# Kernel tuning notes

Measured on AMD Instinct MI355X. Metric: run time of the kernel, lower is better.

The kernel has to match this reference:

```python
import jax, jax.numpy as jnp
from jax import lax
import numpy as np

# ViT-Base / Violin config
P = 16; IMG = 224; C = 768; H = 12; DEPTH = 12
S = 14; NPATCH = S * S            # 196
N = NPATCH + 1                    # 197 with cls token
HID = 4 * C; NCLS = 1000; BATCH = 32
NUM_CURVES = 6
EPS = 1e-5


def _curve_inv_indices(S):
    """Inverse permutations (patch position -> position along curve) for the 6 curves.
    's'  = row-wise snake (boustrophedon), 'h' = column-wise snake, 'm' = anti-diagonal zigzag;
    '*r' = reversed traversal. (Original repo's compute_curve_order helpers were not in the
    provided source; these are faithful stand-ins with the same structure: permutations of 0..195.)"""
    NP_ = S * S
    grid = np.arange(NP_).reshape(S, S)
    orders = {}
    snake = grid.copy(); snake[1::2] = snake[1::2, ::-1]
    orders['s'] = snake.reshape(-1)
    col = grid.T.copy(); col[1::2] = col[1::2, ::-1]
    orders['h'] = col.reshape(-1)
    diag = []
    for d in range(2 * S - 1):
        coords = [(i, d - i) for i in range(max(0, d - S + 1), min(d, S - 1) + 1)]
        if d % 2:
            coords = coords[::-1]
        diag += [grid[i, j] for i, j in coords]
    orders['m'] = np.array(diag)
    for c in ['s', 'h', 'm']:
        orders[c + 'r'] = orders[c][::-1].copy()
    inv = []
    for c in ['s', 'sr', 'h', 'hr', 'm', 'mr']:
        v = np.empty(NP_, np.int32)
        v[orders[c]] = np.arange(NP_, dtype=np.int32)
        inv.append(v)
    return np.stack(inv)  # (6, 196)


def _layernorm(x, w, b):
    m = jnp.mean(x, axis=-1, keepdims=True)
    v = jnp.mean(jnp.square(x - m), axis=-1, keepdims=True)
    return (x - m) / jnp.sqrt(v + EPS) * w + b


def setup_inputs() -> dict:
    key = jax.random.key(0)
    ks = jax.random.split(key, 24)
    rn = lambda k, sh: jax.random.normal(k, sh, jnp.float32) * 0.02
    d = {}
    d["images"] = jax.random.normal(ks[0], (BATCH, 3, IMG, IMG), jnp.float32)
    d["patch_w"] = rn(ks[1], (C, 3, P, P))
    d["patch_b"] = jnp.zeros((C,), jnp.float32)
    d["cls_token"] = rn(ks[2], (1, 1, C))
    d["pos_embed"] = rn(ks[3], (1, N, C))
    d["ln1_w"] = jnp.ones((DEPTH, C), jnp.float32)
    d["ln1_b"] = jnp.zeros((DEPTH, C), jnp.float32)
    d["qkv_w"] = rn(ks[4], (DEPTH, C, 3 * C))   # qkv_bias=False
    d["proj_w"] = rn(ks[5], (DEPTH, C, C))
    d["proj_b"] = jnp.zeros((DEPTH, C), jnp.float32)
    d["ai"] = jax.random.normal(ks[6], (DEPTH, NUM_CURVES, H), jnp.float32)  # torch.randn init
    d["ln2_w"] = jnp.ones((DEPTH, C), jnp.float32)
    d["ln2_b"] = jnp.zeros((DEPTH, C), jnp.float32)
    d["fc1_w"] = rn(ks[7], (DEPTH, C, HID))
    d["fc1_b"] = jnp.zeros((DEPTH, HID), jnp.float32)
    d["fc2_w"] = rn(ks[8], (DEPTH, HID, C))
    d["fc2_b"] = jnp.zeros((DEPTH, C), jnp.float32)
    d["norm_w"] = jnp.ones((C,), jnp.float32)
    d["norm_b"] = jnp.zeros((C,), jnp.float32)
    d["head_w"] = rn(ks[9], (C, NCLS))
    d["head_b"] = jnp.zeros((NCLS,), jnp.float32)
    d["curve_idx"] = jnp.asarray(_curve_inv_indices(S))  # int32 (6, 196)
    return d


def reference(images, patch_w, patch_b, cls_token, pos_embed,
              ln1_w, ln1_b, qkv_w, proj_w, proj_b, ai,
              ln2_w, ln2_b, fc1_w, fc1_b, fc2_w, fc2_b,
              norm_w, norm_b, head_w, head_b, curve_idx):
    B = images.shape[0]
    hd = C // H
    scale = hd ** -0.5
    # patch embed: Conv2d(3, C, k=16, s=16)
    x = lax.conv_general_dilated(images, patch_w, (P, P), 'VALID',
                                 dimension_numbers=('NCHW', 'OIHW', 'NCHW'))
    x = x + patch_b[None, :, None, None]
    x = x.reshape(B, C, NPATCH).transpose(0, 2, 1)          # (B, 196, C)
    x = jnp.concatenate([jnp.broadcast_to(cls_token, (B, 1, C)), x], axis=1)
    x = x + pos_embed                                        # (B, 197, C)

    # curve-distance tensors: |pos_c(p) - pos_c(q)| for each curve c -> (6, 196, 196)
    Dmat = jnp.abs(curve_idx[:, :, None] - curve_idx[:, None, :]).astype(jnp.float32)

    def block(x, p):
        l1w, l1b, qw, pw, pb, a, l2w, l2b, f1w, f1b, f2w, f2b = p
        h = _layernorm(x, l1w, l1b)
        qkv = (h @ qw).reshape(B, N, 3, H, hd).transpose(2, 0, 3, 1, 4)
        q, k, v = qkv[0], qkv[1], qkv[2]                     # (B, H, N, hd)
        attn = jnp.einsum('bhnd,bhmd->bhnm', q, k) * scale
        # multi-curve sigmoid-decay mask, averaged over curves
        sig = jax.nn.sigmoid(a)                              # (6, H)
        core = jnp.power(sig[:, :, None, None], Dmat[:, None, :, :]).mean(0)  # (H,196,196)
        M = jnp.ones((H, N, N), x.dtype).at[:, 1:, 1:].set(core)  # ones for cls row/col
        attn = jax.nn.softmax(attn * M[None], axis=-1)
        o = jnp.einsum('bhnm,bhmd->bhnd', attn, v)
        o = o.transpose(0, 2, 1, 3).reshape(B, N, C)
        x = x + o @ pw + pb
        h2 = _layernorm(x, l2w, l2b)
        h2 = jax.nn.gelu(h2 @ f1w + f1b, approximate=False) @ f2w + f2b
        return x + h2, None

    params = (ln1_w, ln1_b, qkv_w, proj_w, proj_b, ai,
              ln2_w, ln2_b, fc1_w, fc1_b, fc2_w, fc2_b)
    x, _ = lax.scan(block, x, params)
    x = _layernorm(x, norm_w, norm_b)
    return x[:, 0] @ head_w + head_b                          # (B, 1000)
```

## Files before the change

### kernel.cpp

```cpp
#include <hip/hip_runtime.h>
#include <hip/hip_bf16.h>

typedef unsigned int u32;
typedef unsigned short u16;
typedef __attribute__((ext_vector_type(8))) short sh8;
typedef __attribute__((ext_vector_type(4))) float f4;

#define B_   32
#define C_   768
#define H_   12
#define N_   197
#define NP_  196
#define S_   14
#define HID_ 3072
#define NCLS_ 1000
#define ROWS_ (B_ * N_)
#define PROWS_ (B_ * NP_)
#define NT_   13
#define NPAD_ 200

#define AS1(p) ((const __attribute__((address_space(1))) void*)(p))
#define AS3(p) ((__attribute__((address_space(3))) void*)(p))

__device__ __forceinline__ bool probe_bf16(const u32* p) { return p[0] == 0x3F803F80u; }

__device__ __forceinline__ float ldg_any(const void* p, long i, bool isbf) {
    return isbf ? __bfloat162float(((const __hip_bfloat16*)p)[i])
                : ((const float*)p)[i];
}
__device__ __forceinline__ float bfbits2f(u16 u) { return __uint_as_float(((u32)u) << 16); }
__device__ __forceinline__ u16 f2bfbits(float f) {
    __hip_bfloat16 h = __float2bfloat16(f);
    return *(u16*)&h;
}
__device__ __forceinline__ sh8 zero8() {
    sh8 z;
#pragma unroll
    for (int e = 0; e < 8; ++e) z[e] = 0;
    return z;
}

__global__ __launch_bounds__(256)
void im2col_k(const void* __restrict__ images, u16* __restrict__ out, const u32* probe) {
    bool isbf = probe_bf16(probe);
    long idx = (long)blockIdx.x * 256 + threadIdx.x;
    if (idx >= (long)PROWS_ * 768) return;
    int r = (int)(idx / 768), k = (int)(idx % 768);
    int b = r / NP_, p = r % NP_;
    int py = p / S_, px = p % S_;
    int ch = k / 256, rr = k % 256, ii = rr / 16, jj = rr % 16;
    long src = ((long)(b * 3 + ch) * 224 + (py * 16 + ii)) * 224 + (px * 16 + jj);
    out[idx] = f2bfbits(ldg_any(images, src, isbf));
}

__global__ __launch_bounds__(256)
void cast_k(const void* __restrict__ src, u16* __restrict__ dst, long n, const u32* probe) {
    bool isbf = probe_bf16(probe);
    long idx = (long)blockIdx.x * 256 + threadIdx.x;
    if (idx >= n) return;
    dst[idx] = f2bfbits(ldg_any(src, idx, isbf));
}

__global__ __launch_bounds__(256)
void transpose_k(const void* __restrict__ W, long w_off, int K, int N,
                 u16* __restrict__ out, const u32* probe) {
    bool isbf = probe_bf16(probe);
    __shared__ float tile[32][33];
    int tx = threadIdx.x & 31, ty = threadIdx.x >> 5;
    int n0 = blockIdx.x * 32, k0 = blockIdx.y * 32;
#pragma unroll
    for (int i = ty; i < 32; i += 8) {
        int k = k0 + i, n = n0 + tx;
        tile[i][tx] = (k < K && n < N) ? ldg_any(W, w_off + (long)k * N + n, isbf) : 0.f;
    }
    __syncthreads();
#pragma unroll
    for (int i = ty; i < 32; i += 8) {
        int n = n0 + i, k = k0 + tx;
        if (n < N && k < K) out[(long)n * K + k] = f2bfbits(tile[tx][i]);
    }
}

__global__ __launch_bounds__(256)
void cls_k(const void* __restrict__ cls, const void* __restrict__ pos,
           float* __restrict__ x, const u32* probe) {
    bool isbf = probe_bf16(probe);
    int idx = blockIdx.x * 256 + threadIdx.x;
    if (idx >= B_ * C_) return;
    int b = idx / C_, c = idx % C_;
    x[(long)b * N_ * C_ + c] = ldg_any(cls, c, isbf) + ldg_any(pos, c, isbf);
}

__global__ __launch_bounds__(256)
void gemm_bf16_k(const u16* __restrict__ A, int M, int K,
                 const u16* __restrict__ Bt, int N,
                 const void* __restrict__ bias, long bias_off, int has_bias,
                 void* __restrict__ Cp, int ldc, int epi,
                 const void* __restrict__ pos, const u32* __restrict__ probe) {
    __shared__ __align__(16) u16 As[128 * 64];
    __shared__ __align__(16) u16 Bs[128 * 64];
    const int tid = threadIdx.x;
    const int lane = tid & 63, wave = tid >> 6;
    const int wr = (wave >> 1) * 64, wc = (wave & 1) * 64;
    const int m0 = blockIdx.y * 128, n0 = blockIdx.x * 128;
    const int lm = lane & 15, quad = lane >> 4;

    const u16* ga[4];
    const u16* gb[4];
#pragma unroll
    for (int i = 0; i < 4; ++i) {
        int p = i * 256 + tid;
        int r = p >> 3, cslot = p & 7;
        int c = cslot ^ (r & 7);
        int ar = m0 + r; if (ar >= M) ar = M - 1;
        ga[i] = A  + (size_t)ar * K + c * 8;
        gb[i] = Bt + (size_t)(n0 + r) * K + c * 8;
    }

    f4 acc[4][4];
#pragma unroll
    for (int i = 0; i < 4; ++i)
#pragma unroll
        for (int j = 0; j < 4; ++j)
#pragma unroll
            for (int r = 0; r < 4; ++r) acc[i][j][r] = 0.f;

    for (int k0 = 0; k0 < K; k0 += 64) {
        __syncthreads();
#pragma unroll
        for (int i = 0; i < 4; ++i) {
            int p = i * 256 + tid;
            __builtin_amdgcn_global_load_lds(AS1(ga[i] + k0), AS3(As + p * 8), 16, 0, 0);
            __builtin_amdgcn_global_load_lds(AS1(gb[i] + k0), AS3(Bs + p * 8), 16, 0, 0);
        }
        __syncthreads();
#pragma unroll
        for (int ks = 0; ks < 2; ++ks) {
            sh8 af[4], bfv[4];
#pragma unroll
            for (int i = 0; i < 4; ++i) {
                int row = wr + i * 16 + lm;
                int ch = ks * 4 + quad;
                af[i] = *(const sh8*)(As + row * 64 + ((ch ^ (row & 7)) << 3));
                int col = wc + i * 16 + lm;
                bfv[i] = *(const sh8*)(Bs + col * 64 + ((ch ^ (col & 7)) << 3));
            }
#pragma unroll
            for (int i = 0; i < 4; ++i)
#pragma unroll
                for (int j = 0; j < 4; ++j)
                    acc[i][j] = __builtin_amdgcn_mfma_f32_16x16x32_bf16(af[i], bfv[j], acc[i][j], 0, 0, 0);
        }
    }

    const bool isbf = probe_bf16(probe);
#pragma unroll
    for (int j = 0; j < 4; ++j) {
        int col = n0 + wc + j * 16 + lm;
        float bv = has_bias ? ldg_any(bias, bias_off + col, isbf) : 0.f;
#pragma unroll
        for (int i = 0; i < 4; ++i) {
            int rbase = m0 + wr + i * 16 + quad * 4;
#pragma unroll
            for (int r = 0; r < 4; ++r) {
                int row = rbase + r;
                if (row >= M) continue;
                float v = acc[i][j][r] + bv;
                if (epi == 0) {
                    ((u16*)Cp)[(size_t)row * ldc + col] = f2bfbits(v);
                } else if (epi == 1) {
                    v = 0.5f * v * (1.f + erff(v * 0.70710678118654752f));
                    ((u16*)Cp)[(size_t)row * ldc + col] = f2bfbits(v);
                } else if (epi == 2) {
                    ((float*)Cp)[(size_t)row * ldc + col] += v;
                } else {
                    int b = row / NP_, p = row % NP_;
                    v += ldg_any(pos, (long)(1 + p) * C_ + col, isbf);
                    ((float*)Cp)[((size_t)b * N_ + 1 + p) * ldc + col] = v;
                }
            }
        }
    }
}

__global__ __launch_bounds__(256)
void ln_bf16_k(const float* __restrict__ x,
               const void* __restrict__ w, long w_off,
               const void* __restrict__ b, long b_off,
               u16* __restrict__ out, const u32* __restrict__ probe) {
    bool isbf = probe_bf16(probe);
    int lane = threadIdx.x & 63, wave = threadIdx.x >> 6;
    int row = blockIdx.x * 4 + wave;
    const float* xr = x + (size_t)row * C_;
    f4 v[3];
#pragma unroll
    for (int p = 0; p < 3; ++p) v[p] = *(const f4*)(xr + p * 256 + lane * 4);
    float s = 0.f, q = 0.f;
#pragma unroll
    for (int p = 0; p < 3; ++p)
#pragma unroll
        for (int e = 0; e < 4; ++e) { float t = v[p][e]; s += t; q += t * t; }
#pragma unroll
    for (int m = 32; m > 0; m >>= 1) { s += __shfl_xor(s, m); q += __shfl_xor(q, m); }
    float mean = s * (1.f / 768.f);
    float var = q * (1.f / 768.f) - mean * mean;
    float rstd = rsqrtf(var + 1e-5f);
    u16* orow = out + (size_t)row * C_;
#pragma unroll
    for (int p = 0; p < 3; ++p) {
        ushort4 ov;
        int c = p * 256 + lane * 4;
        ov.x = f2bfbits((v[p][0] - mean) * rstd * ldg_any(w, w_off + c + 0, isbf) + ldg_any(b, b_off + c + 0, isbf));
        ov.y = f2bfbits((v[p][1] - mean) * rstd * ldg_any(w, w_off + c + 1, isbf) + ldg_any(b, b_off + c + 1, isbf));
        ov.z = f2bfbits((v[p][2] - mean) * rstd * ldg_any(w, w_off + c + 2, isbf) + ldg_any(b, b_off + c + 2, isbf));
        ov.w = f2bfbits((v[p][3] - mean) * rstd * ldg_any(w, w_off + c + 3, isbf) + ldg_any(b, b_off + c + 3, isbf));
        *(ushort4*)(orow + c) = ov;
    }
}

__global__ __launch_bounds__(256)
void ln_k(const float* __restrict__ x, int row_stride,
          const void* __restrict__ w, long w_off,
          const void* __restrict__ b, long b_off,
          float* __restrict__ out, const u32* __restrict__ probe) {
    bool isbf = probe_bf16(probe);
    int tid = threadIdx.x;
    long row = (long)blockIdx.x * row_stride;
    const float* xr = x + row * C_;
    float v0 = xr[tid], v1 = xr[tid + 256], v2 = xr[tid + 512];
    __shared__ float rs[256], rq[256];
    rs[tid] = v0 + v1 + v2;
    rq[tid] = v0 * v0 + v1 * v1 + v2 * v2;
    __syncthreads();
    for (int st = 128; st > 0; st >>= 1) {
        if (tid < st) { rs[tid] += rs[tid + st]; rq[tid] += rq[tid + st]; }
        __syncthreads();
    }
    float mean = rs[0] * (1.f / 768.f);
    float var = rq[0] * (1.f / 768.f) - mean * mean;
    float rstd = rsqrtf(var + 1e-5f);
    float* orow = out + (long)blockIdx.x * C_;
    orow[tid]       = (v0 - mean) * rstd * ldg_any(w, w_off + tid, isbf)       + ldg_any(b, b_off + tid, isbf);
    orow[tid + 256] = (v1 - mean) * rstd * ldg_any(w, w_off + tid + 256, isbf) + ldg_any(b, b_off + tid + 256, isbf);
    orow[tid + 512] = (v2 - mean) * rstd * ldg_any(w, w_off + tid + 512, isbf) + ldg_any(b, b_off + tid + 512, isbf);
}

__global__ __launch_bounds__(256)
void mask_k(const void* __restrict__ ai, long ai_off, const int* __restrict__ ci,
            float* __restrict__ Mm, const u32* __restrict__ probe) {
    bool isbf = probe_bf16(probe);
    const int h = blockIdx.y;
    __shared__ float ls_s[6];
    __shared__ float pw[6][196];
    if (threadIdx.x < 6) {
        float a = ldg_any(ai, ai_off + threadIdx.x * H_ + h, isbf);
        ls_s[threadIdx.x] = logf(1.f / (1.f + expf(-a)));
    }
    __syncthreads();
    for (int idx = threadIdx.x; idx < 6 * 196; idx += 256) {
        int c = idx / 196, d = idx % 196;
        pw[c][d] = expf((float)d * ls_s[c]);
    }
    __syncthreads();
    int r = blockIdx.x * 256 + threadIdx.x;
    if (r >= N_ * N_) return;
    int i = r / N_, j = r % N_;
    float v;
    if (i == 0 || j == 0) {
        v = 0.125f;
    } else {
        float acc = 0.f;
#pragma unroll
        for (int c = 0; c < 6; ++c) {
            int D = abs(ci[c * NP_ + (i - 1)] - ci[c * NP_ + (j - 1)]);
            acc += pw[c][D];
        }
        v = acc * (0.125f / 6.f);
    }
    Mm[(size_t)h * N_ * N_ + r] = v;
}

__global__ __launch_bounds__(128)
void attn3_k(const u16* __restrict__ qkv, const float* __restrict__ Mm,
             u16* __restrict__ o) {
    __shared__ __align__(16) u16 Ks[208 * 64];
    __shared__ __align__(16) u16 Vt[64 * NPAD_];
    __shared__ __align__(16) u16 Ps[2 * 16 * NPAD_];
    const int h = blockIdx.x, b = blockIdx.y, tid = threadIdx.x;
    const int lane = tid & 63, wave = tid >> 6;
    const int lm = lane & 15, quad = lane >> 4;
    const size_t qkv_b = (size_t)b * N_ * 2304;

    for (int idx = tid; idx < 208 * 8; idx += 128) {
        int r = idx >> 3, c = idx & 7;
        uint4 kv = make_uint4(0u, 0u, 0u, 0u);
        if (r < N_) kv = *(const uint4*)(qkv + qkv_b + (size_t)r * 2304 + 768 + h * 64 + c * 8);
        *(uint4*)(Ks + r * 64 + ((c ^ (r & 7)) << 3)) = kv;
    }
#pragma unroll
    for (int rr = 0; rr < 2; ++rr) {
        int r = tid + rr * 128;
        if (r < NPAD_) {
            ushort vv[64];
            if (r < N_) {
                const u16* vsrc = qkv + qkv_b + (size_t)r * 2304 + 1536 + h * 64;
#pragma unroll
                for (int c = 0; c < 8; ++c) *(uint4*)&vv[c * 8] = *(const uint4*)(vsrc + c * 8);
            } else {
#pragma unroll
                for (int e = 0; e < 64; ++e) vv[e] = 0;
            }
#pragma unroll
            for (int d = 0; d < 64; ++d) Vt[d * NPAD_ + r] = vv[d];
        }
    }
    __syncthreads();

    u16* psw = Ps + wave * 16 * NPAD_;
    for (int rt = wave; rt < NT_; rt += 2) {
        sh8 qf[2];
        int qrow = rt * 16 + lm;
#pragma unroll
        for (int ks = 0; ks < 2; ++ks) {
            qf[ks] = (qrow < N_)
                ? *(const sh8*)(qkv + qkv_b + (size_t)qrow * 2304 + h * 64 + ks * 32 + quad * 8)
                : zero8();
        }
        f4 sacc[NT_];
#pragma unroll
        for (int ct = 0; ct < NT_; ++ct)
#pragma unroll
            for (int r = 0; r < 4; ++r) sacc[ct][r] = 0.f;
#pragma unroll
        for (int ct = 0; ct < NT_; ++ct) {
#pragma unroll
            for (int ks = 0; ks < 2; ++ks) {
                int krow = ct * 16 + lm;
                sh8 kf = *(const sh8*)(Ks + krow * 64 + (((ks * 4 + quad) ^ (krow & 7)) << 3));
                sacc[ct] = __builtin_amdgcn_mfma_f32_16x16x32_bf16(qf[ks], kf, sacc[ct], 0, 0, 0);
            }
        }
        float mx[4] = {-1e30f, -1e30f, -1e30f, -1e30f};
#pragma unroll
        for (int ct = 0; ct < NT_; ++ct) {
            int col = ct * 16 + lm;
            int colc = col < N_ ? col : N_ - 1;
#pragma unroll
            for (int r = 0; r < 4; ++r) {
                int row = rt * 16 + quad * 4 + r;
                int rowc = row < N_ ? row : N_ - 1;
                float mval = Mm[((size_t)h * N_ + rowc) * N_ + colc];
                float v = sacc[ct][r] * mval;
                if (col >= N_) v = -1e30f;
                sacc[ct][r] = v;
                mx[r] = fmaxf(mx[r], v);
            }
        }
#pragma unroll
        for (int m = 8; m > 0; m >>= 1)
#pragma unroll
            for (int r = 0; r < 4; ++r) mx[r] = fmaxf(mx[r], __shfl_xor(mx[r], m));
        float sm[4] = {0.f, 0.f, 0.f, 0.f};
#pragma unroll
        for (int ct = 0; ct < NT_; ++ct) {
            int col = ct * 16 + lm;
#pragma unroll
            for (int r = 0; r < 4; ++r) {
                float p = __expf(sacc[ct][r] - mx[r]);
                sm[r] += p;
                if (col < NPAD_) psw[(quad * 4 + r) * NPAD_ + col] = f2bfbits(p);
            }
        }
#pragma unroll
        for (int m = 8; m > 0; m >>= 1)
#pragma unroll
            for (int r = 0; r < 4; ++r) sm[r] += __shfl_xor(sm[r], m);
        float rden[4];
#pragma unroll
        for (int r = 0; r < 4; ++r) rden[r] = 1.f / sm[r];

        sh8 pf[7];
#pragma unroll
        for (int ms = 0; ms < 7; ++ms) {
            int cm = ms * 4 + quad;
            pf[ms] = (cm <= 24) ? *(const sh8*)(psw + lm * NPAD_ + cm * 8) : zero8();
        }
        f4 oacc[4];
#pragma unroll
        for (int dt = 0; dt < 4; ++dt)
#pragma unroll
            for (int r = 0; r < 4; ++r) oacc[dt][r] = 0.f;
#pragma unroll
        for (int dt = 0; dt < 4; ++dt) {
#pragma unroll
            for (int ms = 0; ms < 7; ++ms) {
                int cm = ms * 4 + quad;
                sh8 vf = (cm <= 24) ? *(const sh8*)(Vt + (dt * 16 + lm) * NPAD_ + cm * 8) : zero8();
                oacc[dt] = __builtin_amdgcn_mfma_f32_16x16x32_bf16(pf[ms], vf, oacc[dt], 0, 0, 0);
            }
        }
#pragma unroll
        for (int dt = 0; dt < 4; ++dt) {
#pragma unroll
            for (int r = 0; r < 4; ++r) {
                int row = rt * 16 + quad * 4 + r;
                if (row < N_)
                    o[((size_t)(b * N_) + row) * C_ + h * 64 + dt * 16 + lm] =
                        f2bfbits(oacc[dt][r] * rden[r]);
            }
        }
    }
}

__global__ __launch_bounds__(256)
void head_k(const float* __restrict__ A,
            const void* __restrict__ W,
            const void* __restrict__ bias,
            void* __restrict__ out, const u32* __restrict__ probe) {
    const bool isbf = probe_bf16(probe);
    const int m = blockIdx.y;
    const int n = blockIdx.x * 256 + threadIdx.x;
    __shared__ float a_s[C_];
    for (int k = threadIdx.x; k < C_; k += 256) a_s[k] = A[(long)m * C_ + k];
    __syncthreads();
    if (n >= NCLS_) return;
    float acc = 0.f;
    if (isbf) {
        const u16* Wb = (const u16*)W;
#pragma unroll 16
        for (int k = 0; k < C_; ++k) acc = fmaf(a_s[k], bfbits2f(Wb[(long)k * NCLS_ + n]), acc);
        acc += bfbits2f(((const u16*)bias)[n]);
        ((u16*)out)[(long)m * NCLS_ + n] = f2bfbits(acc);
    } else {
        const float* Wf = (const float*)W;
#pragma unroll 16
        for (int k = 0; k < C_; ++k) acc = fmaf(a_s[k], Wf[(long)k * NCLS_ + n], acc);
        acc += ((const float*)bias)[n];
        ((float*)out)[(long)m * NCLS_ + n] = acc;
    }
}

extern "C" void kernel_launch(void* const* d_in, const int* in_sizes, int n_in,
                              void* d_out, int out_size, void* d_ws, size_t ws_size,
                              hipStream_t stream) {
    const void* images  = d_in[0];
    const void* patch_w = d_in[1];
    const void* patch_b = d_in[2];
    const void* cls_tok = d_in[3];
    const void* pos_emb = d_in[4];
    const void* ln1_w   = d_in[5];
    const void* ln1_b   = d_in[6];
    const void* qkv_w   = d_in[7];
    const void* proj_w  = d_in[8];
    const void* proj_b  = d_in[9];
    const void* ai      = d_in[10];
    const void* ln2_w   = d_in[11];
    const void* ln2_b   = d_in[12];
    const void* fc1_w   = d_in[13];
    const void* fc1_b   = d_in[14];
    const void* fc2_w   = d_in[15];
    const void* fc2_b   = d_in[16];
    const void* norm_w  = d_in[17];
    const void* norm_b  = d_in[18];
    const void* head_w  = d_in[19];
    const void* head_b  = d_in[20];
    const int*  curve   = (const int*)d_in[21];
    const u32*  probe   = (const u32*)ln1_w;

    char* wsp = (char*)d_ws;
    size_t off = 0;
    auto alloc = [&](size_t bytes) -> void* {
        void* p = wsp + off;
        off += (bytes + 255) & ~(size_t)255;
        return p;
    };
    float* x    = (float*)alloc((size_t)ROWS_ * C_ * 4);
    u16*   hbuf = (u16*)alloc((size_t)ROWS_ * C_ * 2);
    u16*   big  = (u16*)alloc((size_t)ROWS_ * HID_ * 2);
    u16*   obuf = (u16*)alloc((size_t)ROWS_ * C_ * 2);
    float* mm   = (float*)alloc((size_t)H_ * N_ * N_ * 4);
    u16*   wT   = (u16*)alloc((size_t)HID_ * C_ * 2);
    u16*   pwT  = (u16*)alloc((size_t)C_ * C_ * 2);
    float* lnf  = (float*)alloc((size_t)B_ * C_ * 4);
    (void)ws_size; (void)in_sizes; (void)n_in; (void)out_size;

    const int MT = (ROWS_ + 127) / 128;

    im2col_k<<<((long)PROWS_ * 768 + 255) / 256, 256, 0, stream>>>(images, hbuf, probe);
    cast_k<<<(768 * 768 + 255) / 256, 256, 0, stream>>>(patch_w, pwT, (long)768 * 768, probe);
    cls_k<<<(B_ * C_ + 255) / 256, 256, 0, stream>>>(cls_tok, pos_emb, x, probe);
    {
        dim3 g(768 / 128, PROWS_ / 128);
        gemm_bf16_k<<<g, 256, 0, stream>>>(hbuf, PROWS_, 768, pwT, 768,
                                           patch_b, 0, 1, x, 768, 3, pos_emb, probe);
    }

    for (int l = 0; l < 12; ++l) {
        ln_bf16_k<<<ROWS_ / 4, 256, 0, stream>>>(x, ln1_w, (long)l * C_, ln1_b, (long)l * C_, hbuf, probe);
        transpose_k<<<dim3(2304 / 32, 768 / 32), 256, 0, stream>>>(qkv_w, (long)l * 768 * 2304, 768, 2304, wT, probe);
        {
            dim3 g(2304 / 128, MT);
            gemm_bf16_k<<<g, 256, 0, stream>>>(hbuf, ROWS_, 768, wT, 2304,
                                               nullptr, 0, 0, big, 2304, 0, nullptr, probe);
        }
        mask_k<<<dim3((N_ * N_ + 255) / 256, H_), 256, 0, stream>>>(ai, (long)l * 6 * H_, curve, mm, probe);
        attn3_k<<<dim3(H_, B_), 128, 0, stream>>>(big, mm, obuf);
        transpose_k<<<dim3(768 / 32, 768 / 32), 256, 0, stream>>>(proj_w, (long)l * 768 * 768, 768, 768, wT, probe);
        {
            dim3 g(768 / 128, MT);
            gemm_bf16_k<<<g, 256, 0, stream>>>(obuf, ROWS_, 768, wT, 768,
                                               proj_b, (long)l * 768, 1, x, 768, 2, nullptr, probe);
        }
        ln_bf16_k<<<ROWS_ / 4, 256, 0, stream>>>(x, ln2_w, (long)l * C_, ln2_b, (long)l * C_, hbuf, probe);
        transpose_k<<<dim3(3072 / 32, 768 / 32), 256, 0, stream>>>(fc1_w, (long)l * 768 * 3072, 768, 3072, wT, probe);
        {
            dim3 g(3072 / 128, MT);
            gemm_bf16_k<<<g, 256, 0, stream>>>(hbuf, ROWS_, 768, wT, 3072,
                                               fc1_b, (long)l * HID_, 1, big, 3072, 1, nullptr, probe);
        }
        transpose_k<<<dim3(768 / 32, 3072 / 32), 256, 0, stream>>>(fc2_w, (long)l * 3072 * 768, 3072, 768, wT, probe);
        {
            dim3 g(768 / 128, MT);
            gemm_bf16_k<<<g, 256, 0, stream>>>(big, ROWS_, 3072, wT, 768,
                                               fc2_b, (long)l * C_, 1, x, 768, 2, nullptr, probe);
        }
    }

    ln_k<<<B_, 256, 0, stream>>>(x, N_, norm_w, 0, norm_b, 0, lnf, probe);
    head_k<<<dim3((NCLS_ + 255) / 256, B_), 256, 0, stream>>>(lnf, head_w, head_b, d_out, probe);
}
```

Measured before the change: 4.629 ms.

## Double-buffer GEMM LDS tiles and remap workgroups across XCDs

The bf16 GEMM kernel now uses two LDS buffers for the A and B tiles. It prefetches the next K-slice with global_load_lds while MFMAs run on the current slice, so one of the two barriers per iteration is gone and load latency overlaps with compute. The workgroup index is also remapped so that consecutive tiles land on the same XCD, which should improve L2 reuse of shared A/B panels. The cost is twice the LDS per block (64 KB), which may lower occupancy.

```diff
diff --git a/kernel.cpp b/kernel.cpp
--- a/kernel.cpp
+++ b/kernel.cpp
@@ -97,12 +97,19 @@
                  const void* __restrict__ bias, long bias_off, int has_bias,
                  void* __restrict__ Cp, int ldc, int epi,
                  const void* __restrict__ pos, const u32* __restrict__ probe) {
-    __shared__ __align__(16) u16 As[128 * 64];
-    __shared__ __align__(16) u16 Bs[128 * 64];
+    __shared__ __align__(16) u16 As[2][128 * 64];
+    __shared__ __align__(16) u16 Bs[2][128 * 64];
     const int tid = threadIdx.x;
     const int lane = tid & 63, wave = tid >> 6;
     const int wr = (wave >> 1) * 64, wc = (wave & 1) * 64;
-    const int m0 = blockIdx.y * 128, n0 = blockIdx.x * 128;
+
+    const int gx = gridDim.x;
+    const int nwg = gx * gridDim.y;
+    const int lin = blockIdx.y * gx + blockIdx.x;
+    const int q = nwg >> 3, r8 = nwg & 7;
+    const int xcd = lin & 7, cidx = lin >> 3;
+    const int wgid = (xcd < r8 ? xcd * (q + 1) : r8 * (q + 1) + (xcd - r8) * q) + cidx;
+    const int m0 = (wgid / gx) * 128, n0 = (wgid % gx) * 128;
     const int lm = lane & 15, quad = lane >> 4;
 
     const u16* ga[4];
@@ -125,15 +132,26 @@
 #pragma unroll
             for (int r = 0; r < 4; ++r) acc[i][j][r] = 0.f;
 
+#pragma unroll
+    for (int i = 0; i < 4; ++i) {
+        int p = i * 256 + tid;
+        __builtin_amdgcn_global_load_lds(AS1(ga[i]), AS3(&As[0][p * 8]), 16, 0, 0);
+        __builtin_amdgcn_global_load_lds(AS1(gb[i]), AS3(&Bs[0][p * 8]), 16, 0, 0);
+    }
+
+    int cur = 0;
     for (int k0 = 0; k0 < K; k0 += 64) {
         __syncthreads();
-#pragma unroll
-        for (int i = 0; i < 4; ++i) {
-            int p = i * 256 + tid;
-            __builtin_amdgcn_global_load_lds(AS1(ga[i] + k0), AS3(As + p * 8), 16, 0, 0);
-            __builtin_amdgcn_global_load_lds(AS1(gb[i] + k0), AS3(Bs + p * 8), 16, 0, 0);
-        }
-        __syncthreads();
+        if (k0 + 64 < K) {
+#pragma unroll
+            for (int i = 0; i < 4; ++i) {
+                int p = i * 256 + tid;
+                __builtin_amdgcn_global_load_lds(AS1(ga[i] + k0 + 64), AS3(&As[cur ^ 1][p * 8]), 16, 0, 0);
+                __builtin_amdgcn_global_load_lds(AS1(gb[i] + k0 + 64), AS3(&Bs[cur ^ 1][p * 8]), 16, 0, 0);
+            }
+        }
+        const u16* Ac = As[cur];
+        const u16* Bc = Bs[cur];
 #pragma unroll
         for (int ks = 0; ks < 2; ++ks) {
             sh8 af[4], bfv[4];
@@ -141,9 +159,9 @@
             for (int i = 0; i < 4; ++i) {
                 int row = wr + i * 16 + lm;
                 int ch = ks * 4 + quad;
-                af[i] = *(const sh8*)(As + row * 64 + ((ch ^ (row & 7)) << 3));
+                af[i] = *(const sh8*)(Ac + row * 64 + ((ch ^ (row & 7)) << 3));
                 int col = wc + i * 16 + lm;
-                bfv[i] = *(const sh8*)(Bs + col * 64 + ((ch ^ (col & 7)) << 3));
+                bfv[i] = *(const sh8*)(Bc + col * 64 + ((ch ^ (col & 7)) << 3));
             }
 #pragma unroll
             for (int i = 0; i < 4; ++i)
@@ -151,6 +169,7 @@
                 for (int j = 0; j < 4; ++j)
                     acc[i][j] = __builtin_amdgcn_mfma_f32_16x16x32_bf16(af[i], bfv[j], acc[i][j], 0, 0, 0);
         }
+        cur ^= 1;
     }
 
     const bool isbf = probe_bf16(probe);
```

Result: no change. 4.575 ms (-1.2%).

## Batch weight transposes across layers and remap GEMM workgroups per XCD

Applied to the files above, without the earlier changes.

When the workspace is large enough, all 12 layers' weights are transposed and cast to bf16 up front with four 3D-grid launches, replacing the 48 per-layer transpose launches. Each layer's GEMM then reads its own pre-transposed slice. Separately, the GEMM now remaps its linear block index so consecutive tiles land on the same XCD, which is meant to improve L2 reuse. The cost is extra workspace, with a fallback to the old per-layer path when the workspace is too small.

```diff
diff --git a/kernel.cpp b/kernel.cpp
--- a/kernel.cpp
+++ b/kernel.cpp
@@ -82,6 +82,29 @@
 }
 
 __global__ __launch_bounds__(256)
+void transpose_all_k(const void* __restrict__ W, long lstride, int K, int N,
+                     u16* __restrict__ out, const u32* probe) {
+    bool isbf = probe_bf16(probe);
+    __shared__ float tile[32][33];
+    const int l = blockIdx.z;
+    const long w_off = (long)l * lstride;
+    u16* o = out + (long)l * (long)K * N;
+    int tx = threadIdx.x & 31, ty = threadIdx.x >> 5;
+    int n0 = blockIdx.x * 32, k0 = blockIdx.y * 32;
+#pragma unroll
+    for (int i = ty; i < 32; i += 8) {
+        int k = k0 + i, n = n0 + tx;
+        tile[i][tx] = (k < K && n < N) ? ldg_any(W, w_off + (long)k * N + n, isbf) : 0.f;
+    }
+    __syncthreads();
+#pragma unroll
+    for (int i = ty; i < 32; i += 8) {
+        int n = n0 + i, k = k0 + tx;
+        if (n < N && k < K) o[(long)n * K + k] = f2bfbits(tile[tx][i]);
+    }
+}
+
+__global__ __launch_bounds__(256)
 void cls_k(const void* __restrict__ cls, const void* __restrict__ pos,
            float* __restrict__ x, const u32* probe) {
     bool isbf = probe_bf16(probe);
@@ -102,7 +125,14 @@
     const int tid = threadIdx.x;
     const int lane = tid & 63, wave = tid >> 6;
     const int wr = (wave >> 1) * 64, wc = (wave & 1) * 64;
-    const int m0 = blockIdx.y * 128, n0 = blockIdx.x * 128;
+
+    const int gx = gridDim.x;
+    const int nwg = gx * gridDim.y;
+    const int lin = blockIdx.y * gx + blockIdx.x;
+    const int q = nwg >> 3, r8 = nwg & 7;
+    const int xcd = lin & 7, cidx = lin >> 3;
+    const int wgid = (xcd < r8 ? xcd * (q + 1) : r8 * (q + 1) + (xcd - r8) * q) + cidx;
+    const int m0 = (wgid / gx) * 128, n0 = (wgid % gx) * 128;
     const int lm = lane & 15, quad = lane >> 4;
 
     const u16* ga[4];
@@ -482,7 +512,19 @@
     u16*   wT   = (u16*)alloc((size_t)HID_ * C_ * 2);
     u16*   pwT  = (u16*)alloc((size_t)C_ * C_ * 2);
     float* lnf  = (float*)alloc((size_t)B_ * C_ * 4);
-    (void)ws_size; (void)in_sizes; (void)n_in; (void)out_size;
+
+    const size_t qkvT_sz  = (size_t)12 * 2304 * 768;
+    const size_t projT_sz = (size_t)12 * 768 * 768;
+    const size_t fc1T_sz  = (size_t)12 * 3072 * 768;
+    const size_t fc2T_sz  = (size_t)12 * 768 * 3072;
+    size_t off_backup = off;
+    u16* qkvT  = (u16*)alloc(qkvT_sz * 2);
+    u16* projT = (u16*)alloc(projT_sz * 2);
+    u16* fc1T  = (u16*)alloc(fc1T_sz * 2);
+    u16* fc2T  = (u16*)alloc(fc2T_sz * 2);
+    const bool batched = (off <= ws_size);
+    if (!batched) off = off_backup;
+    (void)in_sizes; (void)n_in; (void)out_size;
 
     const int MT = (ROWS_ + 127) / 128;
 
@@ -495,33 +537,49 @@
                                            patch_b, 0, 1, x, 768, 3, pos_emb, probe);
     }
 
+    if (batched) {
+        transpose_all_k<<<dim3(2304 / 32, 768 / 32, 12), 256, 0, stream>>>(qkv_w,  (long)768 * 2304, 768, 2304, qkvT,  probe);
+        transpose_all_k<<<dim3(768 / 32,  768 / 32, 12), 256, 0, stream>>>(proj_w, (long)768 * 768,  768, 768,  projT, probe);
+        transpose_all_k<<<dim3(3072 / 32, 768 / 32, 12), 256, 0, stream>>>(fc1_w,  (long)768 * 3072, 768, 3072, fc1T,  probe);
+        transpose_all_k<<<dim3(768 / 32, 3072 / 32, 12), 256, 0, stream>>>(fc2_w,  (long)3072 * 768, 3072, 768, fc2T,  probe);
+    }
+
     for (int l = 0; l < 12; ++l) {
+        const u16* wq = batched ? qkvT  + (size_t)l * 2304 * 768 : wT;
+        const u16* wp = batched ? projT + (size_t)l * 768 * 768  : wT;
+        const u16* w1 = batched ? fc1T  + (size_t)l * 3072 * 768 : wT;
+        const u16* w2 = batched ? fc2T  + (size_t)l * 768 * 3072 : wT;
+
         ln_bf16_k<<<ROWS_ / 4, 256, 0, stream>>>(x, ln1_w, (long)l * C_, ln1_b, (long)l * C_, hbuf, probe);
-        transpose_k<<<dim3(2304 / 32, 768 / 32), 256, 0, stream>>>(qkv_w, (long)l * 768 * 2304, 768, 2304, wT, probe);
+        if (!batched)
+            transpose_k<<<dim3(2304 / 32, 768 / 32), 256, 0, stream>>>(qkv_w, (long)l * 768 * 2304, 768, 2304, wT, probe);
         {
             dim3 g(2304 / 128, MT);
-            gemm_bf16_k<<<g, 256, 0, stream>>>(hbuf, ROWS_, 768, wT, 2304,
+            gemm_bf16_k<<<g, 256, 0, stream>>>(hbuf, ROWS_, 768, wq, 2304,
                                                nullptr, 0, 0, big, 2304, 0, nullptr, probe);
         }
         mask_k<<<dim3((N_ * N_ + 255) / 256, H_), 256, 0, stream>>>(ai, (long)l * 6 * H_, curve, mm, probe);
         attn3_k<<<dim3(H_, B_), 128, 0, stream>>>(big, mm, obuf);
-        transpose_k<<<dim3(768 / 32, 768 / 32), 256, 0, stream>>>(proj_w, (long)l * 768 * 768, 768, 768, wT, probe);
+        if (!batched)
+            transpose_k<<<dim3(768 / 32, 768 / 32), 256, 0, stream>>>(proj_w, (long)l * 768 * 768, 768, 768, wT, probe);
         {
             dim3 g(768 / 128, MT);
-            gemm_bf16_k<<<g, 256, 0, stream>>>(obuf, ROWS_, 768, wT, 768,
+            gemm_bf16_k<<<g, 256, 0, stream>>>(obuf, ROWS_, 768, wp, 768,
                                                proj_b, (long)l * 768, 1, x, 768, 2, nullptr, probe);
         }
         ln_bf16_k<<<ROWS_ / 4, 256, 0, stream>>>(x, ln2_w, (long)l * C_, ln2_b, (long)l * C_, hbuf, probe);
-        transpose_k<<<dim3(3072 / 32, 768 / 32), 256, 0, stream>>>(fc1_w, (long)l * 768 * 3072, 768, 3072, wT, probe);
+        if (!batched)
+            transpose_k<<<dim3(3072 / 32, 768 / 32), 256, 0, stream>>>(fc1_w, (long)l * 768 * 3072, 768, 3072, wT, probe);
         {
             dim3 g(3072 / 128, MT);
-            gemm_bf16_k<<<g, 256, 0, stream>>>(hbuf, ROWS_, 768, wT, 3072,
+            gemm_bf16_k<<<g, 256, 0, stream>>>(hbuf, ROWS_, 768, w1, 3072,
                                                fc1_b, (long)l * HID_, 1, big, 3072, 1, nullptr, probe);
         }
-        transpose_k<<<dim3(768 / 32, 3072 / 32), 256, 0, stream>>>(fc2_w, (long)l * 3072 * 768, 3072, 768, wT, probe);
+        if (!batched)
+            transpose_k<<<dim3(768 / 32, 3072 / 32), 256, 0, stream>>>(fc2_w, (long)l * 3072 * 768, 3072, 768, wT, probe);
         {
             dim3 g(768 / 128, MT);
-            gemm_bf16_k<<<g, 256, 0, stream>>>(big, ROWS_, 3072, wT, 768,
+            gemm_bf16_k<<<g, 256, 0, stream>>>(big, ROWS_, 3072, w2, 768,
                                                fc2_b, (long)l * C_, 1, x, 768, 2, nullptr, probe);
         }
     }
```

Measured after the change: 4.388 ms. 5.2% less time.
